# Performance work log

Hardware: AMD Instinct MI355X
Metric: run time of the kernel (lower is better)

## Reference

```python
import jax, jax.numpy as jnp
import numpy as np

B, T, D, H, C = 8192, 2048, 1, 256, 10


def setup_inputs() -> dict:
    key = jax.random.key(0)
    ks = jax.random.split(key, 10)
    bound = float(np.sqrt(1.0 / H))
    u = lambda k, shape: jax.random.uniform(k, shape, jnp.float32, -bound, bound)
    return {
        "x": jax.random.normal(ks[0], (B, T), jnp.float32),
        "W_gx": u(ks[1], (D, H)), "W_gh": u(ks[2], (H, H)),
        "W_ix": u(ks[3], (D, H)), "W_ih": u(ks[4], (H, H)),
        "W_fx": u(ks[5], (D, H)), "W_fh": u(ks[6], (H, H)),
        "W_ox": u(ks[7], (D, H)), "W_oh": u(ks[8], (H, H)),
        "W_ph": u(ks[9], (H, C)),
        "b_g": jnp.zeros((1, H), jnp.float32),
        "b_i": jnp.zeros((1, H), jnp.float32),
        "b_f": jnp.ones((1, H), jnp.float32),   # forget-gate bias init = 1 as in source
        "b_o": jnp.zeros((1, H), jnp.float32),
        "b_p": jnp.zeros((1, C), jnp.float32),
    }


def reference(x, W_gx, W_gh, W_ix, W_ih, W_fx, W_fh, W_ox, W_oh, W_ph,
              b_g, b_i, b_f, b_o, b_p):
    # x: [B, T]; each timestep is a scalar feature (input_dim = 1).
    def step(carry, x_t):
        h, c = carry                      # [B, H] each
        xs = x_t[:, None]                 # [B, 1]
        g = jnp.tanh(xs @ W_gx + h @ W_gh + b_g)
        i = jax.nn.sigmoid(xs @ W_ix + h @ W_ih + b_i)
        f = jax.nn.sigmoid(xs @ W_fx + h @ W_fh + b_f)
        o = jax.nn.sigmoid(xs @ W_ox + h @ W_oh + b_o)
        c = g * i + c * f
        h = jnp.tanh(c) * o
        return (h, c), None

    h0 = jnp.zeros((x.shape[0], W_gh.shape[0]), x.dtype)
    c0 = jnp.zeros_like(h0)
    (h, _), _ = jax.lax.scan(step, (h0, c0), x.T)  # scan over time: [T, B]
    return h @ W_ph + b_p                          # [B, num_classes]
```

## Files before the change

kernel.cpp:

```cpp
#include <hip/hip_runtime.h>


#define TT 2048
#define HH 256
#define CC 10

typedef _Float16 half8 __attribute__((ext_vector_type(8)));
typedef float float4v __attribute__((ext_vector_type(4)));

#define WRES_OFF  0
#define RING_OFF  65536
#define RING_SLOT 16384
#define HF_OFF    131072
#define BW_OFF    147456
#define WW_OFF    151552
#define XS_OFF    155648
#define LDS_TOTAL 159744

__device__ __forceinline__ float frcp(float v)  { return __builtin_amdgcn_rcpf(v); }
__device__ __forceinline__ float fex2(float v)  { return __builtin_amdgcn_exp2f(v); }
__device__ __forceinline__ float fsig(float v)  { return frcp(1.0f + fex2(-1.442695040888963f * v)); }
__device__ __forceinline__ float ftanh(float v) { return 2.0f * frcp(1.0f + fex2(-2.885390081777927f * v)) - 1.0f; }

__device__ __forceinline__ void stream_issue(const void* g, void* l) {
    __builtin_amdgcn_global_load_lds((const __attribute__((address_space(1))) void*)g,
                                     (__attribute__((address_space(3))) void*)l, 16, 0, 0);
}
#define WAIT_VM4()     asm volatile("s_waitcnt vmcnt(4)" ::: "memory")
#define BARRIER_LGKM() asm volatile("s_waitcnt lgkmcnt(0)\n\ts_barrier" ::: "memory")

__global__ void pack_weights(const float* __restrict__ Wg, const float* __restrict__ Wi,
                             const float* __restrict__ Wf, const float* __restrict__ Wo,
                             _Float16* __restrict__ wsW) {
    int u = blockIdx.x * blockDim.x + threadIdx.x;
    int kk = u >> 12, rem = u & 4095;
    int s = rem >> 8, rem2 = rem & 255;
    int t = rem2 >> 6, lane = rem2 & 63;
    int q = lane >> 4, l15 = lane & 15;
    int jh = s * 16 + l15;
    const float* Wsrc = (t == 0) ? Wg : (t == 1) ? Wi : (t == 2) ? Wf : Wo;
    half8 v;
#pragma unroll
    for (int j = 0; j < 8; ++j) {
        int k = kk * 32 + q * 8 + j;
        v[j] = (_Float16)Wsrc[k * HH + jh];
    }
    ((half8*)wsW)[u] = v;
}

__attribute__((amdgpu_waves_per_eu(2, 2)))
__global__ void __launch_bounds__(512) lstm_main(
    const float* __restrict__ x, const _Float16* __restrict__ wsW,
    const float* __restrict__ Wgx, const float* __restrict__ Wix,
    const float* __restrict__ Wfx, const float* __restrict__ Wox,
    const float* __restrict__ bg, const float* __restrict__ bi,
    const float* __restrict__ bfp, const float* __restrict__ bo,
    const float* __restrict__ Wp, const float* __restrict__ bp,
    float* __restrict__ out)
{
    extern __shared__ char smem[];
    _Float16* hf  = (_Float16*)(smem + HF_OFF);
    float*    bwL = (float*)(smem + BW_OFF);
    float*    wwL = (float*)(smem + WW_OFF);
    float*    xsL = (float*)(smem + XS_OFF);

    const int tid  = threadIdx.x;
    const int wv   = tid >> 6;
    const int lane = tid & 63;
    const int q    = lane >> 4;
    const int l15  = lane & 15;
    const int s0   = wv * 2;
    const int b0   = blockIdx.x * 32;

    for (int i = tid; i < 8192; i += 512) hf[i] = (_Float16)0.f;
    {
        const uint4* src = (const uint4*)wsW;
        uint4* dst = (uint4*)(smem + WRES_OFF);
        for (int i = tid; i < 65536 / 16; i += 512) dst[i] = src[i];
    }
    {
        const float* bptr[4] = { bg, bi, bfp, bo };
        const float* wptr[4] = { Wgx, Wix, Wfx, Wox };
        for (int i = tid; i < 1024; i += 512) {
            int t = i >> 8, j = i & 255;
            bwL[i] = bptr[t][j];
            wwL[i] = wptr[t][j];
        }
    }
    __syncthreads();

    const char* wl = (const char*)wsW + s0 * 4096 + lane * 16;
    char* ringW = smem + RING_OFF + wv * 2048;
    const _Float16* ringR = (const _Float16*)(smem + RING_OFF) + wv * 1024 + lane * 8;

#pragma unroll
    for (int m = 0; m < 3; ++m) {
        const int kk = 1 + (m >> 2), t = m & 3;
#pragma unroll
        for (int sp = 0; sp < 2; ++sp)
            stream_issue(wl + kk * 65536 + sp * 4096 + t * 1024,
                         ringW + (m & 3) * RING_SLOT + sp * 1024);
    }

    float4v cst[2][2];
#pragma unroll
    for (int mt = 0; mt < 2; ++mt)
#pragma unroll
        for (int sp = 0; sp < 2; ++sp) cst[mt][sp] = (float4v){0.f, 0.f, 0.f, 0.f};

    const int wb = wv * 512 + ((l15 >> 3) * 16 + q * 4) * 8 + (l15 & 7);

#define AREAD(kkv, mtv) (*(const half8*)(hf + (mtv) * 4096 + (kkv) * 512 + lane * 8))

#pragma unroll 1
    for (int ts = 0; ts < TT; ++ts) {
        if ((ts & 31) == 0) {
            const int row = tid >> 4;
            const int c2  = (tid & 15) * 2;
            float2 xv2 = *(const float2*)&x[(b0 + row) * TT + ts + c2];
            *(float2*)&xsL[row * 32 + c2] = xv2;
            BARRIER_LGKM();
        }

        float xv[2][4];
#pragma unroll
        for (int mt = 0; mt < 2; ++mt)
#pragma unroll
            for (int r = 0; r < 4; ++r)
                xv[mt][r] = xsL[(mt * 16 + q * 4 + r) * 32 + (ts & 31)];
        float4v acc[2][2][4];
#pragma unroll
        for (int sp = 0; sp < 2; ++sp) {
            const int jj = (s0 + sp) * 16 + l15;
#pragma unroll
            for (int t = 0; t < 4; ++t) {
                const float bb = bwL[t * 256 + jj];
                const float wx = wwL[t * 256 + jj];
#pragma unroll
                for (int mt = 0; mt < 2; ++mt)
#pragma unroll
                    for (int r = 0; r < 4; ++r)
                        acc[mt][sp][t][r] = bb + xv[mt][r] * wx;
            }
        }

        half8 a0, a1;
        {
            a0 = AREAD(0, 0); a1 = AREAD(0, 1);
            const char* lb = smem + WRES_OFF + s0 * 4096 + lane * 16;
#pragma unroll
            for (int sp = 0; sp < 2; ++sp)
#pragma unroll
                for (int t = 0; t < 4; ++t) {
                    half8 bf = *(const half8*)(lb + sp * 4096 + t * 1024);
                    acc[0][sp][t] = __builtin_amdgcn_mfma_f32_16x16x32_f16(a0, bf, acc[0][sp][t], 0, 0, 0);
                    acc[1][sp][t] = __builtin_amdgcn_mfma_f32_16x16x32_f16(a1, bf, acc[1][sp][t], 0, 0, 0);
                }
        }
#pragma unroll
        for (int m = 0; m < 28; ++m) {
            const int kk = 1 + (m >> 2), t = m & 3, slot = m & 3;
            if (t == 0) { a0 = AREAD(kk, 0); a1 = AREAD(kk, 1); }
            WAIT_VM4();
            half8 bf0 = *(const half8*)(ringR + slot * 8192);
            half8 bf1 = *(const half8*)(ringR + slot * 8192 + 512);
            acc[0][0][t] = __builtin_amdgcn_mfma_f32_16x16x32_f16(a0, bf0, acc[0][0][t], 0, 0, 0);
            acc[1][0][t] = __builtin_amdgcn_mfma_f32_16x16x32_f16(a1, bf0, acc[1][0][t], 0, 0, 0);
            acc[0][1][t] = __builtin_amdgcn_mfma_f32_16x16x32_f16(a0, bf1, acc[0][1][t], 0, 0, 0);
            acc[1][1][t] = __builtin_amdgcn_mfma_f32_16x16x32_f16(a1, bf1, acc[1][1][t], 0, 0, 0);
            {
                int n = m + 3; if (n >= 28) n -= 28;
                const int kkn = 1 + (n >> 2), tn = n & 3, sn = n & 3;
#pragma unroll
                for (int sp = 0; sp < 2; ++sp)
                    stream_issue(wl + kkn * 65536 + sp * 4096 + tn * 1024,
                                 ringW + sn * RING_SLOT + sp * 1024);
            }
        }

        _Float16 hn[2][2][4];
#pragma unroll
        for (int mt = 0; mt < 2; ++mt)
#pragma unroll
            for (int sp = 0; sp < 2; ++sp)
#pragma unroll
                for (int r = 0; r < 4; ++r) {
                    float g  = ftanh(acc[mt][sp][0][r]);
                    float ii = fsig (acc[mt][sp][1][r]);
                    float f  = fsig (acc[mt][sp][2][r]);
                    float o  = fsig (acc[mt][sp][3][r]);
                    float cn = g * ii + cst[mt][sp][r] * f;
                    cst[mt][sp][r] = cn;
                    hn[mt][sp][r] = (_Float16)(ftanh(cn) * o);
                }

        BARRIER_LGKM();
#pragma unroll
        for (int mt = 0; mt < 2; ++mt)
#pragma unroll
            for (int sp = 0; sp < 2; ++sp)
#pragma unroll
                for (int r = 0; r < 4; ++r)
                    hf[mt * 4096 + wb + sp * 256 + r * 8] = hn[mt][sp][r];
        BARRIER_LGKM();
    }

#pragma unroll
    for (int rr = 0; rr < 4; ++rr) {
        int b = wv * 4 + rr;
        int mt = b >> 4, m = b & 15;
        float hv[4];
#pragma unroll
        for (int a = 0; a < 4; ++a) {
            int j = lane + a * 64;
            int idx = mt * 4096 + (j >> 5) * 512 + (((j >> 3) & 3) * 16 + m) * 8 + (j & 7);
            hv[a] = (float)hf[idx];
        }
#pragma unroll
        for (int c = 0; c < CC; ++c) {
            float sacc = 0.f;
#pragma unroll
            for (int a = 0; a < 4; ++a) sacc += hv[a] * Wp[(lane + a * 64) * CC + c];
#pragma unroll
            for (int off = 32; off > 0; off >>= 1) sacc += __shfl_xor(sacc, off, 64);
            if (lane == 0) out[(b0 + b) * CC + c] = sacc + bp[c];
        }
    }
}

extern "C" void kernel_launch(void* const* d_in, const int* in_sizes, int n_in,
                              void* d_out, int out_size, void* d_ws, size_t ws_size,
                              hipStream_t stream) {
    (void)in_sizes; (void)n_in; (void)out_size; (void)ws_size;
    const float* x   = (const float*)d_in[0];
    const float* Wgx = (const float*)d_in[1];
    const float* Wgh = (const float*)d_in[2];
    const float* Wix = (const float*)d_in[3];
    const float* Wih = (const float*)d_in[4];
    const float* Wfx = (const float*)d_in[5];
    const float* Wfh = (const float*)d_in[6];
    const float* Wox = (const float*)d_in[7];
    const float* Woh = (const float*)d_in[8];
    const float* Wp  = (const float*)d_in[9];
    const float* bg  = (const float*)d_in[10];
    const float* bi  = (const float*)d_in[11];
    const float* bf  = (const float*)d_in[12];
    const float* bo  = (const float*)d_in[13];
    const float* bp  = (const float*)d_in[14];
    _Float16* wsW = (_Float16*)d_ws;

    pack_weights<<<128, 256, 0, stream>>>(Wgh, Wih, Wfh, Woh, wsW);

    hipFuncSetAttribute((const void*)lstm_main,
                        hipFuncAttributeMaxDynamicSharedMemorySize, LDS_TOTAL);
    lstm_main<<<256, 512, LDS_TOTAL, stream>>>(
        x, wsW, Wgx, Wix, Wfx, Wox, bg, bi, bf, bo, Wp, bp, (float*)d_out);
}
```

Baseline: 12.27 ms.

## Restructure LSTM step: gate-major MFMA order, deeper weight ring, prefetched x tiles

Reorders the per-timestep loop so each gate's accumulation finishes and its activation is applied before the next gate starts, letting transcendental work overlap later MFMAs. The weight-streaming ring is reworked into 7 smaller slots with one 16B load per step and a deeper prefetch distance (vmcnt 5). x tiles are double-buffered and prefetched asynchronously with global_load_lds, which removes the extra barrier every 32 steps. Biases and input weights move to registers, the h operands are loaded for all k up front, and one per-step barrier is dropped by writing h straight after a single barrier. The cost is higher register pressure and tighter barrier/vmcnt ordering assumptions.

```diff
diff --git a/kernel.cpp b/kernel.cpp
--- a/kernel.cpp
+++ b/kernel.cpp
@@ -10,12 +10,10 @@
 
 #define WRES_OFF  0
 #define RING_OFF  65536
-#define RING_SLOT 16384
-#define HF_OFF    131072
-#define BW_OFF    147456
-#define WW_OFF    151552
-#define XS_OFF    155648
-#define LDS_TOTAL 159744
+#define RING_SLOT 8192
+#define HF_OFF    122880
+#define XS_OFF    139264
+#define LDS_TOTAL 147456
 
 __device__ __forceinline__ float frcp(float v)  { return __builtin_amdgcn_rcpf(v); }
 __device__ __forceinline__ float fex2(float v)  { return __builtin_amdgcn_exp2f(v); }
@@ -26,7 +24,7 @@
     __builtin_amdgcn_global_load_lds((const __attribute__((address_space(1))) void*)g,
                                      (__attribute__((address_space(3))) void*)l, 16, 0, 0);
 }
-#define WAIT_VM4()     asm volatile("s_waitcnt vmcnt(4)" ::: "memory")
+#define WAIT_VM5()     asm volatile("s_waitcnt vmcnt(5)" ::: "memory")
 #define BARRIER_LGKM() asm volatile("s_waitcnt lgkmcnt(0)\n\ts_barrier" ::: "memory")
 
 __global__ void pack_weights(const float* __restrict__ Wg, const float* __restrict__ Wi,
@@ -36,13 +34,13 @@
     int kk = u >> 12, rem = u & 4095;
     int s = rem >> 8, rem2 = rem & 255;
     int t = rem2 >> 6, lane = rem2 & 63;
-    int q = lane >> 4, l15 = lane & 15;
+    int qq = lane >> 4, l15 = lane & 15;
     int jh = s * 16 + l15;
     const float* Wsrc = (t == 0) ? Wg : (t == 1) ? Wi : (t == 2) ? Wf : Wo;
     half8 v;
 #pragma unroll
     for (int j = 0; j < 8; ++j) {
-        int k = kk * 32 + q * 8 + j;
+        int k = kk * 32 + qq * 8 + j;
         v[j] = (_Float16)Wsrc[k * HH + jh];
     }
     ((half8*)wsW)[u] = v;
@@ -59,10 +57,7 @@
     float* __restrict__ out)
 {
     extern __shared__ char smem[];
-    _Float16* hf  = (_Float16*)(smem + HF_OFF);
-    float*    bwL = (float*)(smem + BW_OFF);
-    float*    wwL = (float*)(smem + WW_OFF);
-    float*    xsL = (float*)(smem + XS_OFF);
+    _Float16* hf = (_Float16*)(smem + HF_OFF);
 
     const int tid  = threadIdx.x;
     const int wv   = tid >> 6;
@@ -79,28 +74,35 @@
         for (int i = tid; i < 65536 / 16; i += 512) dst[i] = src[i];
     }
     {
+        float* xs0 = (float*)(smem + XS_OFF);
+        const int row = tid >> 4, c2 = (tid & 15) * 2;
+        float2 xv2 = *(const float2*)&x[(b0 + row) * TT + c2];
+        *(float2*)&xs0[row * 32 + c2] = xv2;
+    }
+    float bbr[4][2], wxr[4][2];
+    {
         const float* bptr[4] = { bg, bi, bfp, bo };
         const float* wptr[4] = { Wgx, Wix, Wfx, Wox };
-        for (int i = tid; i < 1024; i += 512) {
-            int t = i >> 8, j = i & 255;
-            bwL[i] = bptr[t][j];
-            wwL[i] = wptr[t][j];
-        }
+#pragma unroll
+        for (int t = 0; t < 4; ++t)
+#pragma unroll
+            for (int sp = 0; sp < 2; ++sp) {
+                const int jj = (s0 + sp) * 16 + l15;
+                bbr[t][sp] = bptr[t][jj];
+                wxr[t][sp] = wptr[t][jj];
+            }
     }
     __syncthreads();
 
-    const char* wl = (const char*)wsW + s0 * 4096 + lane * 16;
-    char* ringW = smem + RING_OFF + wv * 2048;
-    const _Float16* ringR = (const _Float16*)(smem + RING_OFF) + wv * 1024 + lane * 8;
-
-#pragma unroll
-    for (int m = 0; m < 3; ++m) {
-        const int kk = 1 + (m >> 2), t = m & 3;
-#pragma unroll
-        for (int sp = 0; sp < 2; ++sp)
-            stream_issue(wl + kk * 65536 + sp * 4096 + t * 1024,
-                         ringW + (m & 3) * RING_SLOT + sp * 1024);
-    }
+    const char* wl    = (const char*)wsW + s0 * 4096 + lane * 16;
+    char*       ringW = smem + RING_OFF + wv * 1024;
+    const char* ringR = smem + RING_OFF + wv * 1024 + lane * 16;
+    const char* resB  = smem + WRES_OFF + s0 * 4096 + lane * 16;
+
+#pragma unroll
+    for (int c = 0; c < 6; ++c)
+        stream_issue(wl + (1 + (c >> 1)) * 65536 + (c & 1) * 4096,
+                     ringW + c * RING_SLOT);
 
     float4v cst[2][2];
 #pragma unroll
@@ -109,18 +111,25 @@
         for (int sp = 0; sp < 2; ++sp) cst[mt][sp] = (float4v){0.f, 0.f, 0.f, 0.f};
 
     const int wb = wv * 512 + ((l15 >> 3) * 16 + q * 4) * 8 + (l15 & 7);
-
-#define AREAD(kkv, mtv) (*(const half8*)(hf + (mtv) * 4096 + (kkv) * 512 + lane * 8))
 
 #pragma unroll 1
     for (int ts = 0; ts < TT; ++ts) {
-        if ((ts & 31) == 0) {
-            const int row = tid >> 4;
-            const int c2  = (tid & 15) * 2;
-            float2 xv2 = *(const float2*)&x[(b0 + row) * TT + ts + c2];
-            *(float2*)&xsL[row * 32 + c2] = xv2;
-            BARRIER_LGKM();
-        }
+        if ((ts & 31) == 0 && ts + 32 < TT) {
+            const int w1 = (ts >> 5) + 1;
+            char* xd = smem + XS_OFF + (w1 & 1) * 4096;
+            const float* gx = x + (b0 + (lane >> 3)) * TT + (w1 << 5) + (lane & 7) * 4;
+#pragma unroll
+            for (int j = 0; j < 4; ++j)
+                stream_issue(gx + j * 8 * TT, xd + j * 1024);
+        }
+        const float* xsL = (const float*)(smem + XS_OFF + ((ts >> 5) & 1) * 4096);
+
+        half8 a[8][2];
+#pragma unroll
+        for (int kk = 0; kk < 8; ++kk)
+#pragma unroll
+            for (int mt = 0; mt < 2; ++mt)
+                a[kk][mt] = *(const half8*)(hf + mt * 4096 + kk * 512 + lane * 8);
 
         float xv[2][4];
 #pragma unroll
@@ -128,80 +137,63 @@
 #pragma unroll
             for (int r = 0; r < 4; ++r)
                 xv[mt][r] = xsL[(mt * 16 + q * 4 + r) * 32 + (ts & 31)];
+
+        BARRIER_LGKM();
+
         float4v acc[2][2][4];
 #pragma unroll
-        for (int sp = 0; sp < 2; ++sp) {
-            const int jj = (s0 + sp) * 16 + l15;
-#pragma unroll
-            for (int t = 0; t < 4; ++t) {
-                const float bb = bwL[t * 256 + jj];
-                const float wx = wwL[t * 256 + jj];
+        for (int t = 0; t < 4; ++t) {
+#pragma unroll
+            for (int sp = 0; sp < 2; ++sp)
 #pragma unroll
                 for (int mt = 0; mt < 2; ++mt)
 #pragma unroll
                     for (int r = 0; r < 4; ++r)
-                        acc[mt][sp][t][r] = bb + xv[mt][r] * wx;
+                        acc[mt][sp][t][r] = bbr[t][sp] + xv[mt][r] * wxr[t][sp];
+#pragma unroll
+            for (int sp = 0; sp < 2; ++sp) {
+                half8 bf = *(const half8*)(resB + sp * 4096 + t * 1024);
+                acc[0][sp][t] = __builtin_amdgcn_mfma_f32_16x16x32_f16(a[0][0], bf, acc[0][sp][t], 0, 0, 0);
+                acc[1][sp][t] = __builtin_amdgcn_mfma_f32_16x16x32_f16(a[0][1], bf, acc[1][sp][t], 0, 0, 0);
             }
-        }
-
-        half8 a0, a1;
-        {
-            a0 = AREAD(0, 0); a1 = AREAD(0, 1);
-            const char* lb = smem + WRES_OFF + s0 * 4096 + lane * 16;
+#pragma unroll
+            for (int m = 0; m < 14; ++m) {
+                const int c  = t * 14 + m;
+                const int kk = 1 + (m >> 1), sp = m & 1;
+                WAIT_VM5();
+                half8 bf = *(const half8*)(ringR + (c % 7) * RING_SLOT);
+                acc[0][sp][t] = __builtin_amdgcn_mfma_f32_16x16x32_f16(a[kk][0], bf, acc[0][sp][t], 0, 0, 0);
+                acc[1][sp][t] = __builtin_amdgcn_mfma_f32_16x16x32_f16(a[kk][1], bf, acc[1][sp][t], 0, 0, 0);
+                {
+                    const int n  = (c + 6) % 56;
+                    const int nm = n % 14, nt = n / 14;
+                    stream_issue(wl + (1 + (nm >> 1)) * 65536 + (nm & 1) * 4096 + nt * 1024,
+                                 ringW + (n % 7) * RING_SLOT);
+                }
+            }
 #pragma unroll
             for (int sp = 0; sp < 2; ++sp)
 #pragma unroll
-                for (int t = 0; t < 4; ++t) {
-                    half8 bf = *(const half8*)(lb + sp * 4096 + t * 1024);
-                    acc[0][sp][t] = __builtin_amdgcn_mfma_f32_16x16x32_f16(a0, bf, acc[0][sp][t], 0, 0, 0);
-                    acc[1][sp][t] = __builtin_amdgcn_mfma_f32_16x16x32_f16(a1, bf, acc[1][sp][t], 0, 0, 0);
+                for (int mt = 0; mt < 2; ++mt)
+#pragma unroll
+                    for (int r = 0; r < 4; ++r)
+                        acc[mt][sp][t][r] = (t == 0) ? ftanh(acc[mt][sp][t][r])
+                                                     : fsig(acc[mt][sp][t][r]);
+        }
+
+#pragma unroll
+        for (int mt = 0; mt < 2; ++mt)
+#pragma unroll
+            for (int sp = 0; sp < 2; ++sp)
+#pragma unroll
+                for (int r = 0; r < 4; ++r) {
+                    float cn = acc[mt][sp][0][r] * acc[mt][sp][1][r]
+                             + cst[mt][sp][r]   * acc[mt][sp][2][r];
+                    cst[mt][sp][r] = cn;
+                    hf[mt * 4096 + wb + sp * 256 + r * 8] =
+                        (_Float16)(ftanh(cn) * acc[mt][sp][3][r]);
                 }
-        }
-#pragma unroll
-        for (int m = 0; m < 28; ++m) {
-            const int kk = 1 + (m >> 2), t = m & 3, slot = m & 3;
-            if (t == 0) { a0 = AREAD(kk, 0); a1 = AREAD(kk, 1); }
-            WAIT_VM4();
-            half8 bf0 = *(const half8*)(ringR + slot * 8192);
-            half8 bf1 = *(const half8*)(ringR + slot * 8192 + 512);
-            acc[0][0][t] = __builtin_amdgcn_mfma_f32_16x16x32_f16(a0, bf0, acc[0][0][t], 0, 0, 0);
-            acc[1][0][t] = __builtin_amdgcn_mfma_f32_16x16x32_f16(a1, bf0, acc[1][0][t], 0, 0, 0);
-            acc[0][1][t] = __builtin_amdgcn_mfma_f32_16x16x32_f16(a0, bf1, acc[0][1][t], 0, 0, 0);
-            acc[1][1][t] = __builtin_amdgcn_mfma_f32_16x16x32_f16(a1, bf1, acc[1][1][t], 0, 0, 0);
-            {
-                int n = m + 3; if (n >= 28) n -= 28;
-                const int kkn = 1 + (n >> 2), tn = n & 3, sn = n & 3;
-#pragma unroll
-                for (int sp = 0; sp < 2; ++sp)
-                    stream_issue(wl + kkn * 65536 + sp * 4096 + tn * 1024,
-                                 ringW + sn * RING_SLOT + sp * 1024);
-            }
-        }
-
-        _Float16 hn[2][2][4];
-#pragma unroll
-        for (int mt = 0; mt < 2; ++mt)
-#pragma unroll
-            for (int sp = 0; sp < 2; ++sp)
-#pragma unroll
-                for (int r = 0; r < 4; ++r) {
-                    float g  = ftanh(acc[mt][sp][0][r]);
-                    float ii = fsig (acc[mt][sp][1][r]);
-                    float f  = fsig (acc[mt][sp][2][r]);
-                    float o  = fsig (acc[mt][sp][3][r]);
-                    float cn = g * ii + cst[mt][sp][r] * f;
-                    cst[mt][sp][r] = cn;
-                    hn[mt][sp][r] = (_Float16)(ftanh(cn) * o);
-                }
-
-        BARRIER_LGKM();
-#pragma unroll
-        for (int mt = 0; mt < 2; ++mt)
-#pragma unroll
-            for (int sp = 0; sp < 2; ++sp)
-#pragma unroll
-                for (int r = 0; r < 4; ++r)
-                    hf[mt * 4096 + wb + sp * 256 + r * 8] = hn[mt][sp][r];
+
         BARRIER_LGKM();
     }
 
@@ -211,16 +203,16 @@
         int mt = b >> 4, m = b & 15;
         float hv[4];
 #pragma unroll
-        for (int a = 0; a < 4; ++a) {
-            int j = lane + a * 64;
+        for (int a2 = 0; a2 < 4; ++a2) {
+            int j = lane + a2 * 64;
             int idx = mt * 4096 + (j >> 5) * 512 + (((j >> 3) & 3) * 16 + m) * 8 + (j & 7);
-            hv[a] = (float)hf[idx];
+            hv[a2] = (float)hf[idx];
         }
 #pragma unroll
         for (int c = 0; c < CC; ++c) {
             float sacc = 0.f;
 #pragma unroll
-            for (int a = 0; a < 4; ++a) sacc += hv[a] * Wp[(lane + a * 64) * CC + c];
+            for (int a2 = 0; a2 < 4; ++a2) sacc += hv[a2] * Wp[(lane + a2 * 64) * CC + c];
 #pragma unroll
             for (int off = 32; off > 0; off >>= 1) sacc += __shfl_xor(sacc, off, 64);
             if (lane == 0) out[(b0 + b) * CC + c] = sacc + bp[c];
```

After: 34.18 ms. 2.79x slower.

## Reorder gate GEMM loop gate-major to overlap activations with MFMA

Applied to the files above, without the earlier changes.

Restructures the per-timestep recurrent matmul so each gate (g,i,f,o) is computed fully across all K chunks before moving to the next, changing the weight streaming order to match. The activation (tanh/sigmoid) for each gate is applied right after its accumulation, so transcendental work can overlap with the next gate's MFMAs instead of all running at the end. This reloads the A operand from LDS four times more often and shortens the dependency distance between consecutive MFMAs on the same accumulator.

```diff
diff --git a/kernel.cpp b/kernel.cpp
--- a/kernel.cpp
+++ b/kernel.cpp
@@ -95,11 +95,11 @@
 
 #pragma unroll
     for (int m = 0; m < 3; ++m) {
-        const int kk = 1 + (m >> 2), t = m & 3;
+        const int kk = 1 + m, t = 0;
 #pragma unroll
         for (int sp = 0; sp < 2; ++sp)
             stream_issue(wl + kk * 65536 + sp * 4096 + t * 1024,
-                         ringW + (m & 3) * RING_SLOT + sp * 1024);
+                         ringW + m * RING_SLOT + sp * 1024);
     }
 
     float4v cst[2][2];
@@ -128,12 +128,15 @@
 #pragma unroll
             for (int r = 0; r < 4; ++r)
                 xv[mt][r] = xsL[(mt * 16 + q * 4 + r) * 32 + (ts & 31)];
+
         float4v acc[2][2][4];
-#pragma unroll
-        for (int sp = 0; sp < 2; ++sp) {
-            const int jj = (s0 + sp) * 16 + l15;
-#pragma unroll
-            for (int t = 0; t < 4; ++t) {
+        half8 a0, a1;
+
+#pragma unroll
+        for (int t = 0; t < 4; ++t) {
+#pragma unroll
+            for (int sp = 0; sp < 2; ++sp) {
+                const int jj = (s0 + sp) * 16 + l15;
                 const float bb = bwL[t * 256 + jj];
                 const float wx = wwL[t * 256 + jj];
 #pragma unroll
@@ -142,40 +145,45 @@
                     for (int r = 0; r < 4; ++r)
                         acc[mt][sp][t][r] = bb + xv[mt][r] * wx;
             }
-        }
-
-        half8 a0, a1;
-        {
             a0 = AREAD(0, 0); a1 = AREAD(0, 1);
-            const char* lb = smem + WRES_OFF + s0 * 4096 + lane * 16;
-#pragma unroll
-            for (int sp = 0; sp < 2; ++sp)
-#pragma unroll
-                for (int t = 0; t < 4; ++t) {
+            {
+                const char* lb = smem + WRES_OFF + s0 * 4096 + lane * 16;
+#pragma unroll
+                for (int sp = 0; sp < 2; ++sp) {
                     half8 bf = *(const half8*)(lb + sp * 4096 + t * 1024);
                     acc[0][sp][t] = __builtin_amdgcn_mfma_f32_16x16x32_f16(a0, bf, acc[0][sp][t], 0, 0, 0);
                     acc[1][sp][t] = __builtin_amdgcn_mfma_f32_16x16x32_f16(a1, bf, acc[1][sp][t], 0, 0, 0);
                 }
-        }
-#pragma unroll
-        for (int m = 0; m < 28; ++m) {
-            const int kk = 1 + (m >> 2), t = m & 3, slot = m & 3;
-            if (t == 0) { a0 = AREAD(kk, 0); a1 = AREAD(kk, 1); }
-            WAIT_VM4();
-            half8 bf0 = *(const half8*)(ringR + slot * 8192);
-            half8 bf1 = *(const half8*)(ringR + slot * 8192 + 512);
-            acc[0][0][t] = __builtin_amdgcn_mfma_f32_16x16x32_f16(a0, bf0, acc[0][0][t], 0, 0, 0);
-            acc[1][0][t] = __builtin_amdgcn_mfma_f32_16x16x32_f16(a1, bf0, acc[1][0][t], 0, 0, 0);
-            acc[0][1][t] = __builtin_amdgcn_mfma_f32_16x16x32_f16(a0, bf1, acc[0][1][t], 0, 0, 0);
-            acc[1][1][t] = __builtin_amdgcn_mfma_f32_16x16x32_f16(a1, bf1, acc[1][1][t], 0, 0, 0);
-            {
-                int n = m + 3; if (n >= 28) n -= 28;
-                const int kkn = 1 + (n >> 2), tn = n & 3, sn = n & 3;
-#pragma unroll
-                for (int sp = 0; sp < 2; ++sp)
-                    stream_issue(wl + kkn * 65536 + sp * 4096 + tn * 1024,
-                                 ringW + sn * RING_SLOT + sp * 1024);
             }
+#pragma unroll
+            for (int mm = 0; mm < 7; ++mm) {
+                const int m = t * 7 + mm;
+                const int kk = 1 + mm, slot = m & 3;
+                a0 = AREAD(kk, 0); a1 = AREAD(kk, 1);
+                WAIT_VM4();
+                half8 bf0 = *(const half8*)(ringR + slot * 8192);
+                half8 bf1 = *(const half8*)(ringR + slot * 8192 + 512);
+                acc[0][0][t] = __builtin_amdgcn_mfma_f32_16x16x32_f16(a0, bf0, acc[0][0][t], 0, 0, 0);
+                acc[1][0][t] = __builtin_amdgcn_mfma_f32_16x16x32_f16(a1, bf0, acc[1][0][t], 0, 0, 0);
+                acc[0][1][t] = __builtin_amdgcn_mfma_f32_16x16x32_f16(a0, bf1, acc[0][1][t], 0, 0, 0);
+                acc[1][1][t] = __builtin_amdgcn_mfma_f32_16x16x32_f16(a1, bf1, acc[1][1][t], 0, 0, 0);
+                {
+                    int n = m + 3; if (n >= 28) n -= 28;
+                    const int tn = n / 7, kkn = 1 + (n % 7), sn = n & 3;
+#pragma unroll
+                    for (int sp = 0; sp < 2; ++sp)
+                        stream_issue(wl + kkn * 65536 + sp * 4096 + tn * 1024,
+                                     ringW + sn * RING_SLOT + sp * 1024);
+                }
+            }
+#pragma unroll
+            for (int sp = 0; sp < 2; ++sp)
+#pragma unroll
+                for (int mt = 0; mt < 2; ++mt)
+#pragma unroll
+                    for (int r = 0; r < 4; ++r)
+                        acc[mt][sp][t][r] = (t == 0) ? ftanh(acc[mt][sp][t][r])
+                                                     : fsig(acc[mt][sp][t][r]);
         }
 
         _Float16 hn[2][2][4];
@@ -185,13 +193,10 @@
             for (int sp = 0; sp < 2; ++sp)
 #pragma unroll
                 for (int r = 0; r < 4; ++r) {
-                    float g  = ftanh(acc[mt][sp][0][r]);
-                    float ii = fsig (acc[mt][sp][1][r]);
-                    float f  = fsig (acc[mt][sp][2][r]);
-                    float o  = fsig (acc[mt][sp][3][r]);
-                    float cn = g * ii + cst[mt][sp][r] * f;
+                    float cn = acc[mt][sp][0][r] * acc[mt][sp][1][r]
+                             + cst[mt][sp][r]   * acc[mt][sp][2][r];
                     cst[mt][sp][r] = cn;
-                    hn[mt][sp][r] = (_Float16)(ftanh(cn) * o);
+                    hn[mt][sp][r] = (_Float16)(ftanh(cn) * acc[mt][sp][3][r]);
                 }
 
         BARRIER_LGKM();
@@ -211,16 +216,16 @@
         int mt = b >> 4, m = b & 15;
         float hv[4];
 #pragma unroll
-        for (int a = 0; a < 4; ++a) {
-            int j = lane + a * 64;
+        for (int a2 = 0; a2 < 4; ++a2) {
+            int j = lane + a2 * 64;
             int idx = mt * 4096 + (j >> 5) * 512 + (((j >> 3) & 3) * 16 + m) * 8 + (j & 7);
-            hv[a] = (float)hf[idx];
+            hv[a2] = (float)hf[idx];
         }
 #pragma unroll
         for (int c = 0; c < CC; ++c) {
             float sacc = 0.f;
 #pragma unroll
-            for (int a = 0; a < 4; ++a) sacc += hv[a] * Wp[(lane + a * 64) * CC + c];
+            for (int a2 = 0; a2 < 4; ++a2) sacc += hv[a2] * Wp[(lane + a2 * 64) * CC + c];
 #pragma unroll
             for (int off = 32; off > 0; off >>= 1) sacc += __shfl_xor(sacc, off, 64);
             if (lane == 0) out[(b0 + b) * CC + c] = sacc + bp[c];
```

After: 12.16 ms. Within noise of the previous version (-0.9%).
